# Kernel optimization log

Measured on AMD Instinct MI355X. Metric: run time of the kernel, lower is better.

Reference implementation:

```python
import math
import jax, jax.numpy as jnp
import numpy as np


def _procrustes_R(H):
    # H: [B, 3, 3]. Rotation R = V @ U^T with reflection fix (det(R) >= 0),
    # matching torch.svd convention (v = V, not V^T).
    u, s, vh = jnp.linalg.svd(H)
    v = jnp.swapaxes(vh, -1, -2)                       # [B,3,3]
    r = jnp.einsum('bij,bkj->bik', v, u)               # V @ U^T
    det = jnp.linalg.det(r)                            # [B]
    sign = jnp.where(det < 0, -1.0, 1.0)               # flip last column of V (reflect = diag(1,1,-1))
    flip = jnp.stack([jnp.ones_like(sign), jnp.ones_like(sign), sign], axis=-1)[:, None, :]
    v = v * flip
    return jnp.einsum('bij,bkj->bik', v, u)


def setup_inputs() -> dict:
    key = jax.random.key(0)
    k1, k2, k3, k4 = jax.random.split(key, 4)
    B, D, N, M = 8, 512, 2048, 2048
    return {
        'src_embedding': jax.random.normal(k1, (B, D, N), dtype=jnp.float32),
        'tgt_embedding': jax.random.normal(k2, (B, D, M), dtype=jnp.float32),
        'src': jax.random.normal(k3, (B, 3, N), dtype=jnp.float32),
        'tgt': jax.random.normal(k4, (B, 3, M), dtype=jnp.float32),
    }


def reference(src_embedding, tgt_embedding, src, tgt):
    d_k = src_embedding.shape[1]
    # attention correspondence: scores[b,n,m]
    scores = jnp.einsum('bdn,bdm->bnm', src_embedding, tgt_embedding) / math.sqrt(d_k)
    scores = jax.nn.softmax(scores, axis=2)
    # soft correspondence of src points in tgt: [B,3,N]
    src_corr = jnp.einsum('bdm,bnm->bdn', tgt, scores)
    src_mean = src.mean(axis=2, keepdims=True)          # [B,3,1]
    src_centered = src - src_mean
    src_corr_centered = src_corr - src_corr.mean(axis=2, keepdims=True)
    H = jnp.einsum('bin,bjn->bij', src_centered, src_corr_centered)  # [B,3,3]
    R = _procrustes_R(H)
    t = jnp.einsum('bij,bjk->bik', -R, src_mean) + tgt.mean(axis=2, keepdims=True)
    return R, t.reshape(src.shape[0], 3)
```

## Files before the change

### kernel.cpp

```cpp
#include <hip/hip_runtime.h>
#include <hip/hip_bf16.h>

#define BQ 8
#define DIM 512
#define NN 2048
#define MM 2048

typedef __attribute__((ext_vector_type(8))) short short8;
typedef __attribute__((ext_vector_type(8))) unsigned short ushort8;
typedef __attribute__((ext_vector_type(4))) float floatx4;

#define GLOAD_LDS(gp, lp) \
    __builtin_amdgcn_global_load_lds( \
        (const __attribute__((address_space(1))) void*)(gp), \
        (__attribute__((address_space(3))) void*)(lp), 16, 0, 0)


static __device__ __forceinline__ unsigned short f2bf(float x) {
    __hip_bfloat16 h = __float2bfloat16(x);
    return *(unsigned short*)&h;
}

__global__ __launch_bounds__(256) void transpose_cast_kernel(
    const float* __restrict__ src_emb,
    const float* __restrict__ tgt_emb,
    __hip_bfloat16* __restrict__ Abf,
    __hip_bfloat16* __restrict__ Bbf)
{
    const int n0 = blockIdx.x * 64;
    const int d0 = blockIdx.y * 64;
    const int b  = blockIdx.z & 7;
    const int which = blockIdx.z >> 3;

    const float* in = (which == 0 ? src_emb : tgt_emb) + (size_t)b * DIM * NN;
    __hip_bfloat16* out = (which == 0 ? Abf : Bbf) + (size_t)b * NN * DIM;

    __shared__ float tl[64][65];

    const int t = threadIdx.x;

    {
        const int u = t & 15;
        const int r = t >> 4;
        #pragma unroll
        for (int rr = r; rr < 64; rr += 16) {
            float4 v = *(const float4*)&in[(size_t)(d0 + rr) * NN + n0 + u * 4];
            tl[rr][u * 4 + 0] = v.x;
            tl[rr][u * 4 + 1] = v.y;
            tl[rr][u * 4 + 2] = v.z;
            tl[rr][u * 4 + 3] = v.w;
        }
    }
    __syncthreads();

    {
        const int u = t & 7;
        const int r = t >> 3;
        #pragma unroll
        for (int rn = r; rn < 64; rn += 32) {
            ushort8 o;
            #pragma unroll
            for (int j = 0; j < 8; j++)
                o[j] = f2bf(tl[u * 8 + j][rn]);
            *(ushort8*)&out[(size_t)(n0 + rn) * DIM + d0 + u * 8] = o;
        }
    }
}

__global__ __launch_bounds__(256, 2) void attn_mfma_kernel(
    const __hip_bfloat16* __restrict__ Abf,
    const __hip_bfloat16* __restrict__ Bbf,
    const float* __restrict__ tgt,
    float* __restrict__ part)
{
    const int nt = blockIdx.x;
    const int qt = blockIdx.y;
    const int b  = blockIdx.z;
    const int t  = threadIdx.x;
    const int wave = t >> 6;
    const int lane = t & 63;
    const int lm   = lane & 15;
    const int quad = lane >> 4;
    const int wn   = wave * 32;

    __shared__ short As[128 * 128];
    __shared__ short Bs[128 * 128];

    const __hip_bfloat16* Abase = Abf + ((size_t)(b * NN + nt * 128)) * DIM;
    const int m0 = qt * 128;
    const __hip_bfloat16* Bbase = Bbf + ((size_t)(b * MM + m0)) * DIM;
    const float* Tb = tgt + (size_t)b * 3 * MM;

    const float SCALE = 0.044194173824159216f * 1.4426950408889634f;

    const int lr = lane >> 4;
    const int hh = (lane >> 3) & 1;
    const int c8 = lane & 7;

    floatx4 acc[2][8];
    #pragma unroll
    for (int i = 0; i < 2; i++)
        #pragma unroll
        for (int j = 0; j < 8; j++)
            acc[i][j] = (floatx4){0.f, 0.f, 0.f, 0.f};

    #pragma unroll
    for (int kt = 0; kt < 4; kt++) {
        #pragma unroll
        for (int it = 0; it < 8; it++) {
            const int row = wave * 32 + it * 4 + lr;
            const size_t goff = (size_t)row * DIM + kt * 128 + hh * 64
                              + (c8 ^ (row & 7)) * 8;
            GLOAD_LDS(Abase + goff, &As[(wave * 32 + it * 4) * 128]);
            GLOAD_LDS(Bbase + goff, &Bs[(wave * 32 + it * 4) * 128]);
        }
        __syncthreads();

        #pragma unroll
        for (int ks = 0; ks < 4; ks++) {
            const int col = (ks >> 1) * 64
                          + ((((ks & 1) * 4 + quad) ^ (lm & 7)) * 8);
            short8 af0 = *(const short8*)&As[(wn + lm) * 128 + col];
            short8 af1 = *(const short8*)&As[(wn + 16 + lm) * 128 + col];
            #pragma unroll
            for (int j = 0; j < 8; j++) {
                short8 bf = *(const short8*)&Bs[(j * 16 + lm) * 128 + col];
                acc[0][j] = __builtin_amdgcn_mfma_f32_16x16x32_bf16(af0, bf, acc[0][j], 0, 0, 0);
                acc[1][j] = __builtin_amdgcn_mfma_f32_16x16x32_bf16(af1, bf, acc[1][j], 0, 0, 0);
            }
        }
        __syncthreads();
    }

    float v0[8], v1[8], v2[8];
    #pragma unroll
    for (int j = 0; j < 8; j++) {
        int vc = m0 + j * 16 + lm;
        v0[j] = Tb[vc];
        v1[j] = Tb[MM + vc];
        v2[j] = Tb[2 * MM + vc];
    }

    const size_t slot = (size_t)(b * 16 + qt) * NN;
    #pragma unroll
    for (int i = 0; i < 2; i++) {
        float l4[4] = {0,0,0,0};
        float o0[4] = {0,0,0,0};
        float o1[4] = {0,0,0,0};
        float o2[4] = {0,0,0,0};
        #pragma unroll
        for (int j = 0; j < 8; j++) {
            #pragma unroll
            for (int r = 0; r < 4; r++) {
                float e = __builtin_amdgcn_exp2f(acc[i][j][r] * SCALE);
                l4[r] += e;
                o0[r] += e * v0[j];
                o1[r] += e * v1[j];
                o2[r] += e * v2[j];
            }
        }
        #pragma unroll
        for (int m = 1; m <= 8; m <<= 1) {
            #pragma unroll
            for (int r = 0; r < 4; r++) {
                l4[r] += __shfl_xor(l4[r], m);
                o0[r] += __shfl_xor(o0[r], m);
                o1[r] += __shfl_xor(o1[r], m);
                o2[r] += __shfl_xor(o2[r], m);
            }
        }
        if (lm == 0) {
            #pragma unroll
            for (int r = 0; r < 4; r++) {
                int n = nt * 128 + wn + i * 16 + quad * 4 + r;
                ((float4*)part)[slot + n] = make_float4(l4[r], o0[r], o1[r], o2[r]);
            }
        }
    }
}

__global__ __launch_bounds__(256) void finish_kernel(
    const float* __restrict__ part,
    const float* __restrict__ src,
    const float* __restrict__ tgt,
    float* __restrict__ out)
{
    const int b = blockIdx.x;
    const int t = threadIdx.x;
    const int wave = t >> 6;
    const int lane = t & 63;

    const float4* w4 = (const float4*)part;
    const float* S = src + (size_t)b * 3 * NN;
    const float* T = tgt + (size_t)b * 3 * MM;

    float vals[18];
    #pragma unroll
    for (int c = 0; c < 18; c++) vals[c] = 0.f;

    for (int k = 0; k < 8; k++) {
        const int n = t + k * 256;
        float l = 0.f, y0 = 0.f, y1 = 0.f, y2 = 0.f;
        #pragma unroll
        for (int q = 0; q < 16; q++) {
            float4 p = w4[(size_t)(b * 16 + q) * NN + n];
            l += p.x; y0 += p.y; y1 += p.z; y2 += p.w;
        }
        float inv = 1.0f / l;
        float c0 = y0 * inv, c1 = y1 * inv, c2 = y2 * inv;
        float s0 = S[n], s1 = S[NN + n], s2 = S[2 * NN + n];

        vals[0] += s0;  vals[1] += s1;  vals[2] += s2;
        vals[3] += c0;  vals[4] += c1;  vals[5] += c2;
        vals[6] += T[n]; vals[7] += T[MM + n]; vals[8] += T[2 * MM + n];
        vals[9]  += s0 * c0; vals[10] += s0 * c1; vals[11] += s0 * c2;
        vals[12] += s1 * c0; vals[13] += s1 * c1; vals[14] += s1 * c2;
        vals[15] += s2 * c0; vals[16] += s2 * c1; vals[17] += s2 * c2;
    }

    #pragma unroll
    for (int m = 1; m <= 32; m <<= 1)
        #pragma unroll
        for (int c = 0; c < 18; c++)
            vals[c] += __shfl_xor(vals[c], m);

    __shared__ float wsum[4][18];
    if (lane == 0)
        #pragma unroll
        for (int c = 0; c < 18; c++) wsum[wave][c] = vals[c];
    __syncthreads();

    if (t == 0) {
        float res[18];
        #pragma unroll
        for (int c = 0; c < 18; c++)
            res[c] = wsum[0][c] + wsum[1][c] + wsum[2][c] + wsum[3][c];

        const float invN = 1.0f / (float)NN;
        float mus[3], muc[3], mut[3], H[3][3];
        for (int i = 0; i < 3; i++) {
            mus[i] = res[i] * invN;
            muc[i] = res[3 + i] * invN;
            mut[i] = res[6 + i] * invN;
        }
        for (int i = 0; i < 3; i++)
            for (int j = 0; j < 3; j++)
                H[i][j] = res[9 + i * 3 + j] - (float)NN * mus[i] * muc[j];

        float A[3][3];
        for (int i = 0; i < 3; i++)
            for (int j = 0; j < 3; j++)
                A[i][j] = H[0][i] * H[0][j] + H[1][i] * H[1][j] + H[2][i] * H[2][j];

        float V[3][3] = {{1,0,0},{0,1,0},{0,0,1}};
        for (int sweep = 0; sweep < 6; sweep++) {
            for (int pi = 0; pi < 3; pi++) {
                int p = (pi < 2) ? 0 : 1;
                int q = (pi == 0) ? 1 : 2;
                float apq = A[p][q];
                if (fabsf(apq) < 1e-30f) continue;
                float tau = (A[q][q] - A[p][p]) / (2.0f * apq);
                float tt = (tau >= 0.0f) ? 1.0f / (tau + sqrtf(1.0f + tau * tau))
                                         : -1.0f / (-tau + sqrtf(1.0f + tau * tau));
                float c = 1.0f / sqrtf(1.0f + tt * tt);
                float s = tt * c;
                for (int k = 0; k < 3; k++) {
                    float akp = A[k][p], akq = A[k][q];
                    A[k][p] = c * akp - s * akq;
                    A[k][q] = s * akp + c * akq;
                }
                for (int k = 0; k < 3; k++) {
                    float apk = A[p][k], aqk = A[q][k];
                    A[p][k] = c * apk - s * aqk;
                    A[q][k] = s * apk + c * aqk;
                }
                for (int k = 0; k < 3; k++) {
                    float vkp = V[k][p], vkq = V[k][q];
                    V[k][p] = c * vkp - s * vkq;
                    V[k][q] = s * vkp + c * vkq;
                }
            }
        }

        float lam[3] = {A[0][0], A[1][1], A[2][2]};
        int idx[3] = {0, 1, 2};
        for (int a = 0; a < 2; a++)
            for (int bb = 0; bb < 2 - a; bb++)
                if (lam[idx[bb]] < lam[idx[bb + 1]]) { int tmp = idx[bb]; idx[bb] = idx[bb + 1]; idx[bb + 1] = tmp; }

        float Vc[3][3], U[3][3];
        for (int c = 0; c < 3; c++) {
            float sv = sqrtf(fmaxf(lam[idx[c]], 0.0f));
            float isv = 1.0f / fmaxf(sv, 1e-20f);
            for (int r = 0; r < 3; r++) {
                Vc[r][c] = V[r][idx[c]];
                U[r][c] = (H[r][0] * V[0][idx[c]] + H[r][1] * V[1][idx[c]] + H[r][2] * V[2][idx[c]]) * isv;
            }
        }

        {
            float nrm = rsqrtf(U[0][0]*U[0][0] + U[1][0]*U[1][0] + U[2][0]*U[2][0]);
            for (int r = 0; r < 3; r++) U[r][0] *= nrm;
            float d01 = U[0][0]*U[0][1] + U[1][0]*U[1][1] + U[2][0]*U[2][1];
            for (int r = 0; r < 3; r++) U[r][1] -= d01 * U[r][0];
            nrm = rsqrtf(U[0][1]*U[0][1] + U[1][1]*U[1][1] + U[2][1]*U[2][1]);
            for (int r = 0; r < 3; r++) U[r][1] *= nrm;
            float d02 = U[0][0]*U[0][2] + U[1][0]*U[1][2] + U[2][0]*U[2][2];
            float d12 = U[0][1]*U[0][2] + U[1][1]*U[1][2] + U[2][1]*U[2][2];
            for (int r = 0; r < 3; r++) U[r][2] -= d02 * U[r][0] + d12 * U[r][1];
            nrm = rsqrtf(U[0][2]*U[0][2] + U[1][2]*U[1][2] + U[2][2]*U[2][2]);
            for (int r = 0; r < 3; r++) U[r][2] *= nrm;
        }

        float det = H[0][0]*(H[1][1]*H[2][2] - H[1][2]*H[2][1])
                  - H[0][1]*(H[1][0]*H[2][2] - H[1][2]*H[2][0])
                  + H[0][2]*(H[1][0]*H[2][1] - H[1][1]*H[2][0]);
        float sgn = (det < 0.0f) ? -1.0f : 1.0f;

        float R[3][3];
        for (int i = 0; i < 3; i++)
            for (int j = 0; j < 3; j++)
                R[i][j] = Vc[i][0]*U[j][0] + Vc[i][1]*U[j][1] + sgn * Vc[i][2]*U[j][2];

        for (int i = 0; i < 3; i++)
            for (int j = 0; j < 3; j++)
                out[b * 9 + i * 3 + j] = R[i][j];
        for (int i = 0; i < 3; i++)
            out[BQ * 9 + b * 3 + i] = mut[i] - (R[i][0]*mus[0] + R[i][1]*mus[1] + R[i][2]*mus[2]);
    }
}

extern "C" void kernel_launch(void* const* d_in, const int* in_sizes, int n_in,
                              void* d_out, int out_size, void* d_ws, size_t ws_size,
                              hipStream_t stream) {
    const float* src_emb = (const float*)d_in[0];
    const float* tgt_emb = (const float*)d_in[1];
    const float* src     = (const float*)d_in[2];
    const float* tgt     = (const float*)d_in[3];
    float* out = (float*)d_out;

    float* part = (float*)d_ws;
    __hip_bfloat16* Abf = (__hip_bfloat16*)((char*)d_ws + (4 << 20));
    __hip_bfloat16* Bbf = (__hip_bfloat16*)((char*)d_ws + (20 << 20));

    dim3 gridT(NN / 64, DIM / 64, 2 * BQ);
    transpose_cast_kernel<<<gridT, 256, 0, stream>>>(src_emb, tgt_emb, Abf, Bbf);

    dim3 gridA(NN / 128, MM / 128, BQ);
    attn_mfma_kernel<<<gridA, 256, 0, stream>>>(Abf, Bbf, tgt, part);

    finish_kernel<<<BQ, 256, 0, stream>>>(part, src, tgt, out);
}
```

Baseline: 183.6 us.

## Fuse fp32-to-bf16 transpose cast into attention MFMA kernel with larger N tile

Drops the separate transpose/cast kernel and its bf16 workspace round trip. The attention kernel now reads fp32 embeddings straight from global memory, converts them to bf16 in registers and writes swizzled tiles to LDS. The N tile grows from 128 to 256, giving each wave a 64x128 output block so fewer blocks re-read tgt. In exchange, global loads become scalar fp32 strided per k-row instead of async 16-byte LDS loads, and each block redoes the conversion work (the src tile is recast for each of 16 M tiles), so there is more global traffic and more ALU work per block.

```diff
diff --git a/kernel.cpp b/kernel.cpp
--- a/kernel.cpp
+++ b/kernel.cpp
@@ -7,13 +7,7 @@
 #define MM 2048
 
 typedef __attribute__((ext_vector_type(8))) short short8;
-typedef __attribute__((ext_vector_type(8))) unsigned short ushort8;
 typedef __attribute__((ext_vector_type(4))) float floatx4;
-
-#define GLOAD_LDS(gp, lp) \
-    __builtin_amdgcn_global_load_lds( \
-        (const __attribute__((address_space(1))) void*)(gp), \
-        (__attribute__((address_space(3))) void*)(lp), 16, 0, 0)
 
 
 static __device__ __forceinline__ unsigned short f2bf(float x) {
@@ -21,55 +15,9 @@
     return *(unsigned short*)&h;
 }
 
-__global__ __launch_bounds__(256) void transpose_cast_kernel(
+__global__ __launch_bounds__(256, 2) void attn_fused_kernel(
     const float* __restrict__ src_emb,
     const float* __restrict__ tgt_emb,
-    __hip_bfloat16* __restrict__ Abf,
-    __hip_bfloat16* __restrict__ Bbf)
-{
-    const int n0 = blockIdx.x * 64;
-    const int d0 = blockIdx.y * 64;
-    const int b  = blockIdx.z & 7;
-    const int which = blockIdx.z >> 3;
-
-    const float* in = (which == 0 ? src_emb : tgt_emb) + (size_t)b * DIM * NN;
-    __hip_bfloat16* out = (which == 0 ? Abf : Bbf) + (size_t)b * NN * DIM;
-
-    __shared__ float tl[64][65];
-
-    const int t = threadIdx.x;
-
-    {
-        const int u = t & 15;
-        const int r = t >> 4;
-        #pragma unroll
-        for (int rr = r; rr < 64; rr += 16) {
-            float4 v = *(const float4*)&in[(size_t)(d0 + rr) * NN + n0 + u * 4];
-            tl[rr][u * 4 + 0] = v.x;
-            tl[rr][u * 4 + 1] = v.y;
-            tl[rr][u * 4 + 2] = v.z;
-            tl[rr][u * 4 + 3] = v.w;
-        }
-    }
-    __syncthreads();
-
-    {
-        const int u = t & 7;
-        const int r = t >> 3;
-        #pragma unroll
-        for (int rn = r; rn < 64; rn += 32) {
-            ushort8 o;
-            #pragma unroll
-            for (int j = 0; j < 8; j++)
-                o[j] = f2bf(tl[u * 8 + j][rn]);
-            *(ushort8*)&out[(size_t)(n0 + rn) * DIM + d0 + u * 8] = o;
-        }
-    }
-}
-
-__global__ __launch_bounds__(256, 2) void attn_mfma_kernel(
-    const __hip_bfloat16* __restrict__ Abf,
-    const __hip_bfloat16* __restrict__ Bbf,
     const float* __restrict__ tgt,
     float* __restrict__ part)
 {
@@ -81,52 +29,75 @@
     const int lane = t & 63;
     const int lm   = lane & 15;
     const int quad = lane >> 4;
-    const int wn   = wave * 32;
-
-    __shared__ short As[128 * 128];
-    __shared__ short Bs[128 * 128];
-
-    const __hip_bfloat16* Abase = Abf + ((size_t)(b * NN + nt * 128)) * DIM;
+    const int wn   = wave * 64;
+
+    __shared__ short As[256 * 64];
+    __shared__ short Bs[128 * 64];
+
+    const float* Ab = src_emb + (size_t)b * DIM * NN + nt * 256;
     const int m0 = qt * 128;
-    const __hip_bfloat16* Bbase = Bbf + ((size_t)(b * MM + m0)) * DIM;
+    const float* Bb = tgt_emb + (size_t)b * DIM * MM + m0;
     const float* Tb = tgt + (size_t)b * 3 * MM;
 
     const float SCALE = 0.044194173824159216f * 1.4426950408889634f;
 
-    const int lr = lane >> 4;
-    const int hh = (lane >> 3) & 1;
-    const int c8 = lane & 7;
-
-    floatx4 acc[2][8];
-    #pragma unroll
-    for (int i = 0; i < 2; i++)
+    const int na  = wave * 64 + lane;
+    const int mb  = wave * 32 + (lane & 31);
+    const int bch = lane >> 5;
+
+    floatx4 acc[4][8];
+    #pragma unroll
+    for (int i = 0; i < 4; i++)
         #pragma unroll
         for (int j = 0; j < 8; j++)
             acc[i][j] = (floatx4){0.f, 0.f, 0.f, 0.f};
 
     #pragma unroll
-    for (int kt = 0; kt < 4; kt++) {
-        #pragma unroll
-        for (int it = 0; it < 8; it++) {
-            const int row = wave * 32 + it * 4 + lr;
-            const size_t goff = (size_t)row * DIM + kt * 128 + hh * 64
-                              + (c8 ^ (row & 7)) * 8;
-            GLOAD_LDS(Abase + goff, &As[(wave * 32 + it * 4) * 128]);
-            GLOAD_LDS(Bbase + goff, &Bs[(wave * 32 + it * 4) * 128]);
+    for (int kt = 0; kt < 8; kt++) {
+        #pragma unroll
+        for (int j = 0; j < 8; j++) {
+            float v[8];
+            #pragma unroll
+            for (int jj = 0; jj < 8; jj++)
+                v[jj] = Ab[(size_t)(kt * 64 + j * 8 + jj) * NN + na];
+            unsigned int p[4];
+            #pragma unroll
+            for (int jj = 0; jj < 4; jj++)
+                p[jj] = ((unsigned)f2bf(v[2 * jj + 1]) << 16) | (unsigned)f2bf(v[2 * jj]);
+            const int pc = (j ^ (na & 7)) * 8;
+            uint4 w; w.x = p[0]; w.y = p[1]; w.z = p[2]; w.w = p[3];
+            *(uint4*)&As[na * 64 + pc] = w;
+        }
+        #pragma unroll
+        for (int j2 = 0; j2 < 4; j2++) {
+            const int j = j2 * 2 + bch;
+            float v[8];
+            #pragma unroll
+            for (int jj = 0; jj < 8; jj++)
+                v[jj] = Bb[(size_t)(kt * 64 + j * 8 + jj) * MM + mb];
+            unsigned int p[4];
+            #pragma unroll
+            for (int jj = 0; jj < 4; jj++)
+                p[jj] = ((unsigned)f2bf(v[2 * jj + 1]) << 16) | (unsigned)f2bf(v[2 * jj]);
+            const int pc = (j ^ (mb & 7)) * 8;
+            uint4 w; w.x = p[0]; w.y = p[1]; w.z = p[2]; w.w = p[3];
+            *(uint4*)&Bs[mb * 64 + pc] = w;
         }
         __syncthreads();
 
         #pragma unroll
-        for (int ks = 0; ks < 4; ks++) {
-            const int col = (ks >> 1) * 64
-                          + ((((ks & 1) * 4 + quad) ^ (lm & 7)) * 8);
-            short8 af0 = *(const short8*)&As[(wn + lm) * 128 + col];
-            short8 af1 = *(const short8*)&As[(wn + 16 + lm) * 128 + col];
+        for (int ks = 0; ks < 2; ks++) {
+            const int pc = (((ks * 4 + quad) ^ (lane & 7)) * 8);
+            short8 af[4];
+            #pragma unroll
+            for (int i = 0; i < 4; i++)
+                af[i] = *(const short8*)&As[(wn + i * 16 + lm) * 64 + pc];
             #pragma unroll
             for (int j = 0; j < 8; j++) {
-                short8 bf = *(const short8*)&Bs[(j * 16 + lm) * 128 + col];
-                acc[0][j] = __builtin_amdgcn_mfma_f32_16x16x32_bf16(af0, bf, acc[0][j], 0, 0, 0);
-                acc[1][j] = __builtin_amdgcn_mfma_f32_16x16x32_bf16(af1, bf, acc[1][j], 0, 0, 0);
+                short8 bf = *(const short8*)&Bs[(j * 16 + lm) * 64 + pc];
+                #pragma unroll
+                for (int i = 0; i < 4; i++)
+                    acc[i][j] = __builtin_amdgcn_mfma_f32_16x16x32_bf16(af[i], bf, acc[i][j], 0, 0, 0);
             }
         }
         __syncthreads();
@@ -143,7 +114,7 @@
 
     const size_t slot = (size_t)(b * 16 + qt) * NN;
     #pragma unroll
-    for (int i = 0; i < 2; i++) {
+    for (int i = 0; i < 4; i++) {
         float l4[4] = {0,0,0,0};
         float o0[4] = {0,0,0,0};
         float o1[4] = {0,0,0,0};
@@ -172,7 +143,7 @@
         if (lm == 0) {
             #pragma unroll
             for (int r = 0; r < 4; r++) {
-                int n = nt * 128 + wn + i * 16 + quad * 4 + r;
+                int n = nt * 256 + wn + i * 16 + quad * 4 + r;
                 ((float4*)part)[slot + n] = make_float4(l4[r], o0[r], o1[r], o2[r]);
             }
         }
@@ -340,14 +311,9 @@
     float* out = (float*)d_out;
 
     float* part = (float*)d_ws;
-    __hip_bfloat16* Abf = (__hip_bfloat16*)((char*)d_ws + (4 << 20));
-    __hip_bfloat16* Bbf = (__hip_bfloat16*)((char*)d_ws + (20 << 20));
-
-    dim3 gridT(NN / 64, DIM / 64, 2 * BQ);
-    transpose_cast_kernel<<<gridT, 256, 0, stream>>>(src_emb, tgt_emb, Abf, Bbf);
-
-    dim3 gridA(NN / 128, MM / 128, BQ);
-    attn_mfma_kernel<<<gridA, 256, 0, stream>>>(Abf, Bbf, tgt, part);
+
+    dim3 gridA(NN / 256, MM / 128, BQ);
+    attn_fused_kernel<<<gridA, 256, 0, stream>>>(src_emb, tgt_emb, tgt, part);
 
     finish_kernel<<<BQ, 256, 0, stream>>>(part, src, tgt, out);
 }
```

Result: slower. 209.3 us (+14.0%).
